# Performance work log

Measured on AMD Instinct MI355X. Metric: run time of the kernel, lower is better.

Reference implementation:

```python
import jax, jax.numpy as jnp
import numpy as np

B, N, E = 8, 10000, 320000
IN_DIM, E_H, E_OUT, N_OUT = 16, 32, 22, 16


def setup_inputs() -> dict:
    key = jax.random.key(0)
    ks = jax.random.split(key, 8)
    x = jax.random.uniform(ks[0], (B, N, IN_DIM), dtype=jnp.float32)
    edge_index = jax.random.randint(ks[1], (2, E), 0, N, dtype=jnp.int64)
    # edge_attr: col 0 = city_dist (keep strictly positive), col 1 = city_direc
    ea = jax.random.uniform(ks[2], (E, 2), dtype=jnp.float32)
    edge_attr = jnp.stack([ea[:, 0] * 100.0 + 1.0, ea[:, 1] * 360.0], axis=-1)
    wind_min = jnp.array([0.0, 0.0], dtype=jnp.float32)
    wind_max = jnp.array([15.0, 360.0], dtype=jnp.float32)
    W1 = jax.random.normal(ks[3], (2 * IN_DIM + 2 + 1, E_H), dtype=jnp.float32) * 0.1
    b1 = jnp.zeros((E_H,), dtype=jnp.float32)
    W2 = jax.random.normal(ks[4], (E_H, E_OUT), dtype=jnp.float32) * 0.1
    b2 = jnp.zeros((E_OUT,), dtype=jnp.float32)
    Wn = jax.random.normal(ks[5], (E_OUT, N_OUT), dtype=jnp.float32) * 0.1
    bn = jnp.zeros((N_OUT,), dtype=jnp.float32)
    return {"x": x, "edge_index": edge_index, "edge_attr": edge_attr,
            "wind_min": wind_min, "wind_max": wind_max,
            "W1": W1, "b1": b1, "W2": W2, "b2": b2, "Wn": Wn, "bn": bn}


def reference(x, edge_index, edge_attr, wind_min, wind_max, W1, b1, W2, b2, Wn, bn):
    edge_src = edge_index[0]
    edge_tgt = edge_index[1]
    n_nodes = x.shape[1]

    node_src = x[:, edge_src]      # [B, E, F]
    node_tgt = x[:, edge_tgt]      # [B, E, F]

    # de-normalize the last two features (wind speed, wind direction)
    src_wind = node_src[..., -2:] * (wind_max - wind_min) + wind_min
    src_speed = src_wind[..., 0]   # [B, E]
    src_direc = src_wind[..., 1]   # [B, E]

    city_dist = edge_attr[:, 0]    # [E]
    city_direc = edge_attr[:, 1]   # [E]

    theta = jnp.abs(city_direc[None, :] - src_direc)
    edge_weight = jax.nn.relu(src_speed * jnp.cos(theta) / city_dist[None, :])  # [B, E]

    ea_min = edge_attr.min(axis=0)
    ea_max = edge_attr.max(axis=0)
    ea_norm = (edge_attr - ea_min) / (ea_max - ea_min)  # [E, 2]
    ea_norm_b = jnp.broadcast_to(ea_norm[None], (x.shape[0],) + ea_norm.shape)

    feat = jnp.concatenate([node_src, node_tgt, ea_norm_b, edge_weight[..., None]], axis=-1)  # [B, E, 35]

    h = jax.nn.sigmoid(feat @ W1 + b1)   # [B, E, 32]
    e = jax.nn.sigmoid(h @ W2 + b2)      # [B, E, 22]

    # scatter_add to target nodes, scatter_add of negated messages to source nodes
    agg = jnp.zeros((x.shape[0], n_nodes, e.shape[-1]), dtype=e.dtype)
    agg = agg.at[:, edge_tgt].add(e)
    agg = agg.at[:, edge_src].add(-e)

    return jax.nn.sigmoid(agg @ Wn + bn)  # [B, N, out_dim]
```

## Files before the change

kernel.cpp:

```cpp
#include <hip/hip_runtime.h>
#include <math.h>

#define BB 8
#define NN 10000
#define EE 320000
#define NCHUNK 128
#define CHSZ (EE / NCHUNK)
#define LOG2E 1.44269504088896340736f

#define OFF_MM   0
#define PK_W2P   16
#define PK_WNP   368
#define PK_W1S   544
#define PK_B1S   576
#define PK_B2S   608
#define OFF_WIND 640
#define OFF_ECS  160640
#define OFF_PRE1 800640
#define OFF_PRE2 3360640
#define OFF_OFFP 5920640
#define OFF_TOT  5940642
#define OFF_MMP  5960642
#define OFF_CNTC 5961154
#define OFF_LST  8521154
#define OFF_G    9161168

typedef _Float16 half2_t __attribute__((ext_vector_type(2)));
typedef __fp16 fp16v2_t __attribute__((ext_vector_type(2)));

__device__ __forceinline__ float rcpf(float x) {
#if __has_builtin(__builtin_amdgcn_rcpf)
    return __builtin_amdgcn_rcpf(x);
#else
    return __fdividef(1.0f, x);
#endif
}

__device__ __forceinline__ half2_t pkh2(float a, float b) {
#if __has_builtin(__builtin_amdgcn_cvt_pkrtz)
    union { fp16v2_t t; half2_t h; } u;
    u.t = __builtin_amdgcn_cvt_pkrtz(a, b);
    return u.h;
#else
    half2_t r; r.x = (_Float16)a; r.y = (_Float16)b; return r;
#endif
}

__device__ __forceinline__ float fdot2(half2_t a, half2_t b, float c) {
#if __has_builtin(__builtin_amdgcn_fdot2)
    return __builtin_amdgcn_fdot2(a, b, c, false);
#else
    return (float)a.x * (float)b.x + (float)a.y * (float)b.y + c;
#endif
}

__device__ __forceinline__ float sig2(float xs) {
    return rcpf(1.0f + exp2f(-xs));
}

__device__ __forceinline__ float sigmf(float x) {
    return __fdividef(1.0f, 1.0f + __expf(-x));
}

union h2f { half2_t h; float f; };

__global__ __launch_bounds__(512) void pack_kernel(const float* __restrict__ W1,
                                                   const float* __restrict__ b1,
                                                   const float* __restrict__ W2,
                                                   const float* __restrict__ b2,
                                                   const float* __restrict__ Wn,
                                                   float* __restrict__ ws) {
    int t = threadIdx.x;
    if (t < 352) {
        int j2 = t / 22, k = t % 22;
        h2f u; u.h = pkh2(W2[(2 * j2) * 22 + k] * LOG2E, W2[(2 * j2 + 1) * 22 + k] * LOG2E);
        ws[PK_W2P + t] = u.f;
    }
    if (t < 176) {
        int k2 = t / 16, i = t % 16;
        h2f u; u.h = pkh2(Wn[(2 * k2) * 16 + i], Wn[(2 * k2 + 1) * 16 + i]);
        ws[PK_WNP + t] = u.f;
    }
    if (t < 32) {
        ws[PK_W1S + t] = W1[34 * 32 + t] * LOG2E;
        ws[PK_B1S + t] = b1[t] * LOG2E;
    }
    if (t < 22) ws[PK_B2S + t] = b2[t] * LOG2E;
}

__global__ __launch_bounds__(256) void count_kernel(const int* __restrict__ ei,
                                                    const float* __restrict__ ea,
                                                    unsigned* __restrict__ cntc,
                                                    float* __restrict__ mmpart) {
    __shared__ unsigned hist[NN];
    __shared__ float mred[4][4];
    const int c = blockIdx.x, a = blockIdx.y, tid = threadIdx.x;
    for (int i = tid; i < NN; i += 256) hist[i] = 0u;
    __syncthreads();
    const int e0 = c * CHSZ;
    float n0 = 3.4e38f, n1 = 3.4e38f, x0 = 0.f, x1 = 0.f;
    for (int k = tid; k < CHSZ; k += 256) {
        int v = ei[(size_t)a * EE + e0 + k];
        atomicAdd(&hist[v], 1u);
        if (a == 0) {
            float2 av = ((const float2*)ea)[e0 + k];
            n0 = fminf(n0, av.x); x0 = fmaxf(x0, av.x);
            n1 = fminf(n1, av.y); x1 = fmaxf(x1, av.y);
        }
    }
    __syncthreads();
    unsigned* dst = cntc + ((size_t)a * NCHUNK + c) * NN;
    for (int i = tid; i < NN; i += 256) dst[i] = hist[i];
    if (a == 0) {
        #pragma unroll
        for (int off = 32; off >= 1; off >>= 1) {
            n0 = fminf(n0, __shfl_xor(n0, off)); n1 = fminf(n1, __shfl_xor(n1, off));
            x0 = fmaxf(x0, __shfl_xor(x0, off)); x1 = fmaxf(x1, __shfl_xor(x1, off));
        }
        int w = tid >> 6;
        if ((tid & 63) == 0) { mred[w][0] = n0; mred[w][1] = n1; mred[w][2] = x0; mred[w][3] = x1; }
        __syncthreads();
        if (tid == 0) {
            mmpart[c * 4 + 0] = fminf(fminf(mred[0][0], mred[1][0]), fminf(mred[2][0], mred[3][0]));
            mmpart[c * 4 + 1] = fminf(fminf(mred[0][1], mred[1][1]), fminf(mred[2][1], mred[3][1]));
            mmpart[c * 4 + 2] = fmaxf(fmaxf(mred[0][2], mred[1][2]), fmaxf(mred[2][2], mred[3][2]));
            mmpart[c * 4 + 3] = fmaxf(fmaxf(mred[0][3], mred[1][3]), fmaxf(mred[2][3], mred[3][3]));
        }
    }
}

__global__ __launch_bounds__(256) void tot_kernel(const unsigned* __restrict__ cntc,
                                                  unsigned* __restrict__ tot) {
    int v = blockIdx.x * 256 + threadIdx.x;
    int a = blockIdx.y;
    if (v >= NN) return;
    const unsigned* base = cntc + (size_t)a * NCHUNK * NN;
    unsigned s = 0;
    for (int c = 0; c < NCHUNK; c++) s += base[(size_t)c * NN + v];
    tot[a * NN + v] = s;
}

__global__ __launch_bounds__(1024) void scan_kernel(const unsigned* __restrict__ tot,
                                                    const float* __restrict__ mmpart,
                                                    unsigned* __restrict__ offp,
                                                    float* __restrict__ mmo) {
    __shared__ unsigned ts[1024];
    int t = threadIdx.x;
    if (t < 64) {
        float n0 = fminf(mmpart[4 * t + 0], mmpart[4 * (t + 64) + 0]);
        float n1 = fminf(mmpart[4 * t + 1], mmpart[4 * (t + 64) + 1]);
        float x0 = fmaxf(mmpart[4 * t + 2], mmpart[4 * (t + 64) + 2]);
        float x1 = fmaxf(mmpart[4 * t + 3], mmpart[4 * (t + 64) + 3]);
        #pragma unroll
        for (int off = 32; off >= 1; off >>= 1) {
            n0 = fminf(n0, __shfl_xor(n0, off)); n1 = fminf(n1, __shfl_xor(n1, off));
            x0 = fmaxf(x0, __shfl_xor(x0, off)); x1 = fmaxf(x1, __shfl_xor(x1, off));
        }
        if (t == 0) {
            mmo[0] = n0; mmo[1] = n1;
            mmo[2] = __fdividef(LOG2E, x0 - n0);
            mmo[3] = __fdividef(LOG2E, x1 - n1);
        }
    }
    const int CH = 10;
    for (int a = 0; a < 2; a++) {
        const unsigned* c = tot + a * NN;
        unsigned* off = offp + a * (NN + 1);
        unsigned s = 0;
        int i0 = t * CH;
        #pragma unroll
        for (int k = 0; k < CH; k++) { int i = i0 + k; if (i < NN) s += c[i]; }
        ts[t] = s;
        __syncthreads();
        for (int d = 1; d < 1024; d <<= 1) {
            unsigned v = (t >= d) ? ts[t - d] : 0u;
            __syncthreads();
            ts[t] += v;
            __syncthreads();
        }
        unsigned run = ts[t] - s;
        #pragma unroll
        for (int k = 0; k < CH; k++) {
            int i = i0 + k;
            if (i < NN) { unsigned cv = c[i]; off[i] = run; run += cv; }
        }
        if (t == 1023) off[NN] = ts[1023];
        __syncthreads();
    }
}

__global__ __launch_bounds__(256) void base_kernel(unsigned* __restrict__ cntc,
                                                   const unsigned* __restrict__ offp) {
    int v = blockIdx.x * 256 + threadIdx.x;
    int a = blockIdx.y;
    if (v >= NN) return;
    unsigned run = offp[a * (NN + 1) + v];
    unsigned* base = cntc + (size_t)a * NCHUNK * NN;
    for (int c = 0; c < NCHUNK; c++) {
        unsigned cv = base[(size_t)c * NN + v];
        base[(size_t)c * NN + v] = run;
        run += cv;
    }
}

__global__ __launch_bounds__(256) void fill_kernel(const int* __restrict__ ei,
                                                   const unsigned* __restrict__ cntc,
                                                   unsigned* __restrict__ lst) {
    __shared__ unsigned cur[NN];
    const int c = blockIdx.x, a = blockIdx.y, tid = threadIdx.x;
    const unsigned* bs = cntc + ((size_t)a * NCHUNK + c) * NN;
    for (int i = tid; i < NN; i += 256) cur[i] = bs[i];
    __syncthreads();
    const int e0 = c * CHSZ;
    for (int k = tid; k < CHSZ; k += 256) {
        int e = e0 + k;
        int v = ei[(size_t)a * EE + e];
        unsigned p = atomicAdd(&cur[v], 1u);
        lst[(size_t)a * EE + p] = (unsigned)e;
    }
}

__global__ __launch_bounds__(256) void node_pre(const float* __restrict__ x,
                                                const float* __restrict__ W1,
                                                const float* __restrict__ wmin,
                                                const float* __restrict__ wmax,
                                                float* __restrict__ pre1,
                                                float* __restrict__ pre2,
                                                float* __restrict__ wind) {
    int id = blockIdx.x * 256 + threadIdx.x;
    if (id >= BB * NN) return;
    float xv[16];
    const float4* xp = (const float4*)(x + (size_t)id * 16);
    #pragma unroll
    for (int q = 0; q < 4; q++) {
        float4 v = xp[q];
        xv[4 * q + 0] = v.x; xv[4 * q + 1] = v.y;
        xv[4 * q + 2] = v.z; xv[4 * q + 3] = v.w;
    }
    float s1[32], s2[32];
    #pragma unroll
    for (int j = 0; j < 32; j++) { s1[j] = 0.f; s2[j] = 0.f; }
    #pragma unroll
    for (int r = 0; r < 16; r++) {
        float xr = xv[r];
        #pragma unroll
        for (int j = 0; j < 32; j++) {
            s1[j] = fmaf(xr, W1[r * 32 + j], s1[j]);
            s2[j] = fmaf(xr, W1[(16 + r) * 32 + j], s2[j]);
        }
    }
    float4* o1 = (float4*)(pre1 + (size_t)id * 32);
    float4* o2 = (float4*)(pre2 + (size_t)id * 32);
    #pragma unroll
    for (int q = 0; q < 8; q++) {
        o1[q] = make_float4(s1[4*q] * LOG2E, s1[4*q+1] * LOG2E, s1[4*q+2] * LOG2E, s1[4*q+3] * LOG2E);
        o2[q] = make_float4(s2[4*q] * LOG2E, s2[4*q+1] * LOG2E, s2[4*q+2] * LOG2E, s2[4*q+3] * LOG2E);
    }
    float sp = xv[14] * (wmax[0] - wmin[0]) + wmin[0];
    float dr = xv[15] * (wmax[1] - wmin[1]) + wmin[1];
    float sv, cv;
    sincosf(dr, &sv, &cv);
    ((float2*)wind)[id] = make_float2(sp * cv, sp * sv);
}

__global__ __launch_bounds__(256) void edge_pre(const float* __restrict__ ea,
                                                float* __restrict__ ecs) {
    int e = blockIdx.x * 256 + threadIdx.x;
    float2 av = ((const float2*)ea)[e];
    float sv, cv;
    sincosf(av.y, &sv, &cv);
    float rd = __fdividef(1.0f, av.x);
    ((float2*)ecs)[e] = make_float2(cv * rd, sv * rd);
}

__global__ __launch_bounds__(256) void edge_mlp(const int* __restrict__ ei,
                                                const float* __restrict__ ea,
                                                const float* __restrict__ ecs,
                                                const float* __restrict__ pre1,
                                                const float* __restrict__ pre2,
                                                const float* __restrict__ wind,
                                                const float* __restrict__ mmo,
                                                const float* __restrict__ W1,
                                                const float* __restrict__ wsf,
                                                float* __restrict__ gbuf,
                                                int b0, int nb) {
    __shared__ float gs[256 * 17];

    const int tid = threadIdx.x;
    const int e = blockIdx.x * 256 + tid;
    const int brel = blockIdx.y;
    const int b = b0 + brel;

    const int src = ei[e];
    const int tgt = ei[EE + e];
    const float2 eav = ((const float2*)ea)[e];
    const float2 ec = ((const float2*)ecs)[e];
    const float2 wv = ((const float2*)wind)[(size_t)b * NN + src];

    float ew = fmaxf(wv.x * ec.x + wv.y * ec.y, 0.f);
    float ean0 = (eav.x - mmo[0]) * mmo[2];
    float ean1 = (eav.y - mmo[1]) * mmo[3];

    const float* w1s = wsf + PK_W1S;
    const float* b1s = wsf + PK_B1S;
    const float* b2s = wsf + PK_B2S;
    const half2_t* W2p = (const half2_t*)(wsf + PK_W2P);
    const half2_t* Wnp = (const half2_t*)(wsf + PK_WNP);

    half2_t hp[16];
    const float4* p1 = (const float4*)(pre1 + ((size_t)b * NN + src) * 32);
    const float4* p2 = (const float4*)(pre2 + ((size_t)b * NN + tgt) * 32);
    #pragma unroll
    for (int q = 0; q < 8; q++) {
        float4 a = p1[q];
        float4 c = p2[q];
        float s0 = a.x + c.x, s1 = a.y + c.y, s2 = a.z + c.z, s3 = a.w + c.w;
        float h0, h1, h2, h3;
        {
            int j = 4 * q;
            h0 = sig2(s0 + ean0 * W1[32*32 + j+0] + ean1 * W1[33*32 + j+0] + ew * w1s[j+0] + b1s[j+0]);
            h1 = sig2(s1 + ean0 * W1[32*32 + j+1] + ean1 * W1[33*32 + j+1] + ew * w1s[j+1] + b1s[j+1]);
            h2 = sig2(s2 + ean0 * W1[32*32 + j+2] + ean1 * W1[33*32 + j+2] + ew * w1s[j+2] + b1s[j+2]);
            h3 = sig2(s3 + ean0 * W1[32*32 + j+3] + ean1 * W1[33*32 + j+3] + ew * w1s[j+3] + b1s[j+3]);
        }
        hp[2 * q]     = pkh2(h0, h1);
        hp[2 * q + 1] = pkh2(h2, h3);
    }

    float ef[22];
    #pragma unroll
    for (int k = 0; k < 22; k++) ef[k] = b2s[k];
    #pragma unroll
    for (int j2 = 0; j2 < 16; j2++) {
        #pragma unroll
        for (int k = 0; k < 22; k++) ef[k] = fdot2(hp[j2], W2p[j2 * 22 + k], ef[k]);
    }
    half2_t efp[11];
    #pragma unroll
    for (int k2 = 0; k2 < 11; k2++) {
        float e0 = sig2(ef[2 * k2]);
        float e1 = sig2(ef[2 * k2 + 1]);
        efp[k2] = pkh2(e0, e1);
    }

    float gg[16];
    #pragma unroll
    for (int i = 0; i < 16; i++) gg[i] = 0.f;
    #pragma unroll
    for (int k2 = 0; k2 < 11; k2++) {
        #pragma unroll
        for (int i = 0; i < 16; i++) gg[i] = fdot2(efp[k2], Wnp[k2 * 16 + i], gg[i]);
    }

    #pragma unroll
    for (int i = 0; i < 16; i++) gs[tid * 17 + i] = gg[i];
    __syncthreads();

    const int c = tid & 15;
    const int base = tid >> 4;
    const size_t ebase = (size_t)blockIdx.x * 256;
    #pragma unroll
    for (int p = 0; p < 16; p++) {
        int s = base + p * 16;
        gbuf[((ebase + s) * (size_t)nb + brel) * 16 + c] = gs[s * 17 + c];
    }
}

__global__ __launch_bounds__(256) void gather_kernel(const unsigned* __restrict__ offp,
                                                     const unsigned* __restrict__ lst,
                                                     const float* __restrict__ gbuf,
                                                     const float* __restrict__ bn,
                                                     float* __restrict__ out,
                                                     int b0, int nb, int npb, int lgper) {
    int tid = threadIdx.x;
    int n = blockIdx.x * npb + (tid >> lgper);
    int rem = tid & ((1 << lgper) - 1);
    int bi = rem >> 4;
    int c = rem & 15;

    unsigned s0 = offp[n], s1 = offp[n + 1];
    unsigned t0 = offp[NN + 1 + n], t1 = offp[NN + 1 + n + 1];

    float acc = 0.f;
    for (unsigned k = t0; k < t1; k++) {
        int e = (int)lst[EE + k];
        acc += gbuf[((size_t)e * nb + bi) * 16 + c];
    }
    for (unsigned k = s0; k < s1; k++) {
        int e = (int)lst[k];
        acc -= gbuf[((size_t)e * nb + bi) * 16 + c];
    }
    out[((size_t)(b0 + bi) * NN + n) * 16 + c] = sigmf(acc + bn[c]);
}

extern "C" void kernel_launch(void* const* d_in, const int* in_sizes, int n_in,
                              void* d_out, int out_size, void* d_ws, size_t ws_size,
                              hipStream_t stream) {
    const float* x    = (const float*)d_in[0];
    const int*   ei   = (const int*)d_in[1];
    const float* ea   = (const float*)d_in[2];
    const float* wmin = (const float*)d_in[3];
    const float* wmax = (const float*)d_in[4];
    const float* W1   = (const float*)d_in[5];
    const float* b1   = (const float*)d_in[6];
    const float* W2   = (const float*)d_in[7];
    const float* b2   = (const float*)d_in[8];
    const float* Wn   = (const float*)d_in[9];
    const float* bn   = (const float*)d_in[10];
    float* out = (float*)d_out;

    float* ws       = (float*)d_ws;
    float* mmo      = ws + OFF_MM;
    float* wind     = ws + OFF_WIND;
    float* ecs      = ws + OFF_ECS;
    float* pre1     = ws + OFF_PRE1;
    float* pre2     = ws + OFF_PRE2;
    unsigned* offp  = (unsigned*)(ws + OFF_OFFP);
    unsigned* tot   = (unsigned*)(ws + OFF_TOT);
    float* mmpart   = ws + OFF_MMP;
    unsigned* cntc  = (unsigned*)(ws + OFF_CNTC);
    unsigned* lst   = (unsigned*)(ws + OFF_LST);
    float* gbuf     = ws + OFF_G;

    int nb = 8;
    while (nb > 1 && ((size_t)OFF_G + (size_t)nb * EE * 16) * 4ull > ws_size) nb >>= 1;
    if (((size_t)OFF_G + (size_t)nb * EE * 16) * 4ull > ws_size) return;

    pack_kernel<<<1, 512, 0, stream>>>(W1, b1, W2, b2, Wn, ws);
    node_pre<<<(BB * NN + 255) / 256, 256, 0, stream>>>(x, W1, wmin, wmax, pre1, pre2, wind);
    edge_pre<<<EE / 256, 256, 0, stream>>>(ea, ecs);

    count_kernel<<<dim3(NCHUNK, 2), 256, 0, stream>>>(ei, ea, cntc, mmpart);
    tot_kernel<<<dim3((NN + 255) / 256, 2), 256, 0, stream>>>(cntc, tot);
    scan_kernel<<<1, 1024, 0, stream>>>(tot, mmpart, offp, mmo);
    base_kernel<<<dim3((NN + 255) / 256, 2), 256, 0, stream>>>(cntc, offp);
    fill_kernel<<<dim3(NCHUNK, 2), 256, 0, stream>>>(ei, cntc, lst);

    int lgnb = (nb == 8) ? 3 : (nb == 4) ? 2 : (nb == 2) ? 1 : 0;
    int per = 16 * nb;
    int npb = 256 / per;
    int lgper = 4 + lgnb;
    for (int bc = 0; bc < BB; bc += nb) {
        edge_mlp<<<dim3(EE / 256, nb), 256, 0, stream>>>(ei, ea, ecs, pre1, pre2, wind,
                                                         mmo, W1, ws, gbuf, bc, nb);
        gather_kernel<<<NN / npb, 256, 0, stream>>>(offp, lst, gbuf, bn, out,
                                                    bc, nb, npb, lgper);
    }
}
```

Baseline: 428.6 us.

## Scatter edge messages into CSR-sorted slots and split chunk prefix sums into groups

```diff
diff --git a/kernel.cpp b/kernel.cpp
--- a/kernel.cpp
+++ b/kernel.cpp
@@ -6,6 +6,8 @@
 #define EE 320000
 #define NCHUNK 128
 #define CHSZ (EE / NCHUNK)
+#define NGRP 8
+#define GCH (NCHUNK / NGRP)
 #define LOG2E 1.44269504088896340736f
 
 #define OFF_MM   0
@@ -19,11 +21,12 @@
 #define OFF_PRE1 800640
 #define OFF_PRE2 3360640
 #define OFF_OFFP 5920640
-#define OFF_TOT  5940642
-#define OFF_MMP  5960642
-#define OFF_CNTC 5961154
-#define OFF_LST  8521154
-#define OFF_G    9161168
+#define OFF_MMP  5940642
+#define OFF_TOT8 5941154
+#define OFF_GB   6101154
+#define OFF_CNTC 6261154
+#define OFF_POS  8821154
+#define OFF_S    9461156
 
 typedef _Float16 half2_t __attribute__((ext_vector_type(2)));
 typedef __fp16 fp16v2_t __attribute__((ext_vector_type(2)));
@@ -129,20 +132,22 @@
     }
 }
 
-__global__ __launch_bounds__(256) void tot_kernel(const unsigned* __restrict__ cntc,
-                                                  unsigned* __restrict__ tot) {
+__global__ __launch_bounds__(256) void tot8_kernel(const unsigned* __restrict__ cntc,
+                                                   unsigned* __restrict__ tot8) {
     int v = blockIdx.x * 256 + threadIdx.x;
-    int a = blockIdx.y;
+    int a = blockIdx.y, q = blockIdx.z;
     if (v >= NN) return;
-    const unsigned* base = cntc + (size_t)a * NCHUNK * NN;
+    const unsigned* base = cntc + (size_t)a * NCHUNK * NN + (size_t)q * GCH * NN;
     unsigned s = 0;
-    for (int c = 0; c < NCHUNK; c++) s += base[(size_t)c * NN + v];
-    tot[a * NN + v] = s;
-}
-
-__global__ __launch_bounds__(1024) void scan_kernel(const unsigned* __restrict__ tot,
+    #pragma unroll
+    for (int c = 0; c < GCH; c++) s += base[(size_t)c * NN + v];
+    tot8[(q * 2 + a) * NN + v] = s;
+}
+
+__global__ __launch_bounds__(1024) void scan_kernel(const unsigned* __restrict__ tot8,
                                                     const float* __restrict__ mmpart,
                                                     unsigned* __restrict__ offp,
+                                                    unsigned* __restrict__ gb,
                                                     float* __restrict__ mmo) {
     __shared__ unsigned ts[1024];
     int t = threadIdx.x;
@@ -164,39 +169,54 @@
     }
     const int CH = 10;
     for (int a = 0; a < 2; a++) {
-        const unsigned* c = tot + a * NN;
-        unsigned* off = offp + a * (NN + 1);
+        unsigned tv[CH];
         unsigned s = 0;
         int i0 = t * CH;
-        #pragma unroll
-        for (int k = 0; k < CH; k++) { int i = i0 + k; if (i < NN) s += c[i]; }
+        for (int k = 0; k < CH; k++) {
+            int i = i0 + k;
+            unsigned x = 0;
+            if (i < NN) {
+                #pragma unroll
+                for (int q = 0; q < NGRP; q++) x += tot8[(q * 2 + a) * NN + i];
+            }
+            tv[k] = x; s += x;
+        }
         ts[t] = s;
         __syncthreads();
         for (int d = 1; d < 1024; d <<= 1) {
-            unsigned v = (t >= d) ? ts[t - d] : 0u;
+            unsigned u = (t >= d) ? ts[t - d] : 0u;
             __syncthreads();
-            ts[t] += v;
+            ts[t] += u;
             __syncthreads();
         }
         unsigned run = ts[t] - s;
-        #pragma unroll
         for (int k = 0; k < CH; k++) {
             int i = i0 + k;
-            if (i < NN) { unsigned cv = c[i]; off[i] = run; run += cv; }
-        }
-        if (t == 1023) off[NN] = ts[1023];
+            if (i < NN) {
+                offp[a * (NN + 1) + i] = run;
+                unsigned gq = run;
+                #pragma unroll
+                for (int q = 0; q < NGRP; q++) {
+                    gb[(q * 2 + a) * NN + i] = gq;
+                    gq += tot8[(q * 2 + a) * NN + i];
+                }
+                run += tv[k];
+            }
+        }
+        if (t == 1023) offp[a * (NN + 1) + NN] = ts[1023];
         __syncthreads();
     }
 }
 
 __global__ __launch_bounds__(256) void base_kernel(unsigned* __restrict__ cntc,
-                                                   const unsigned* __restrict__ offp) {
+                                                   const unsigned* __restrict__ gb) {
     int v = blockIdx.x * 256 + threadIdx.x;
-    int a = blockIdx.y;
+    int a = blockIdx.y, q = blockIdx.z;
     if (v >= NN) return;
-    unsigned run = offp[a * (NN + 1) + v];
-    unsigned* base = cntc + (size_t)a * NCHUNK * NN;
-    for (int c = 0; c < NCHUNK; c++) {
+    unsigned run = gb[(q * 2 + a) * NN + v];
+    unsigned* base = cntc + (size_t)a * NCHUNK * NN + (size_t)q * GCH * NN;
+    #pragma unroll
+    for (int c = 0; c < GCH; c++) {
         unsigned cv = base[(size_t)c * NN + v];
         base[(size_t)c * NN + v] = run;
         run += cv;
@@ -205,7 +225,7 @@
 
 __global__ __launch_bounds__(256) void fill_kernel(const int* __restrict__ ei,
                                                    const unsigned* __restrict__ cntc,
-                                                   unsigned* __restrict__ lst) {
+                                                   unsigned* __restrict__ pos) {
     __shared__ unsigned cur[NN];
     const int c = blockIdx.x, a = blockIdx.y, tid = threadIdx.x;
     const unsigned* bs = cntc + ((size_t)a * NCHUNK + c) * NN;
@@ -216,7 +236,7 @@
         int e = e0 + k;
         int v = ei[(size_t)a * EE + e];
         unsigned p = atomicAdd(&cur[v], 1u);
-        lst[(size_t)a * EE + p] = (unsigned)e;
+        pos[(size_t)a * EE + e] = p;
     }
 }
 
@@ -282,9 +302,11 @@
                                                 const float* __restrict__ mmo,
                                                 const float* __restrict__ W1,
                                                 const float* __restrict__ wsf,
-                                                float* __restrict__ gbuf,
+                                                const unsigned* __restrict__ pos,
+                                                float* __restrict__ sbuf,
                                                 int b0, int nb) {
     __shared__ float gs[256 * 17];
+    __shared__ unsigned sl[512];
 
     const int tid = threadIdx.x;
     const int e = blockIdx.x * 256 + tid;
@@ -296,6 +318,8 @@
     const float2 eav = ((const float2*)ea)[e];
     const float2 ec = ((const float2*)ecs)[e];
     const float2 wv = ((const float2*)wind)[(size_t)b * NN + src];
+    sl[tid] = pos[e];
+    sl[256 + tid] = EE + pos[EE + e];
 
     float ew = fmaxf(wv.x * ec.x + wv.y * ec.y, 0.f);
     float ean0 = (eav.x - mmo[0]) * mmo[2];
@@ -358,17 +382,17 @@
 
     const int c = tid & 15;
     const int base = tid >> 4;
-    const size_t ebase = (size_t)blockIdx.x * 256;
     #pragma unroll
     for (int p = 0; p < 16; p++) {
         int s = base + p * 16;
-        gbuf[((ebase + s) * (size_t)nb + brel) * 16 + c] = gs[s * 17 + c];
+        float val = gs[s * 17 + c];
+        sbuf[((size_t)sl[s] * nb + brel) * 16 + c] = -val;
+        sbuf[((size_t)sl[256 + s] * nb + brel) * 16 + c] = val;
     }
 }
 
 __global__ __launch_bounds__(256) void gather_kernel(const unsigned* __restrict__ offp,
-                                                     const unsigned* __restrict__ lst,
-                                                     const float* __restrict__ gbuf,
+                                                     const float* __restrict__ sbuf,
                                                      const float* __restrict__ bn,
                                                      float* __restrict__ out,
                                                      int b0, int nb, int npb, int lgper) {
@@ -382,14 +406,10 @@
     unsigned t0 = offp[NN + 1 + n], t1 = offp[NN + 1 + n + 1];
 
     float acc = 0.f;
-    for (unsigned k = t0; k < t1; k++) {
-        int e = (int)lst[EE + k];
-        acc += gbuf[((size_t)e * nb + bi) * 16 + c];
-    }
-    for (unsigned k = s0; k < s1; k++) {
-        int e = (int)lst[k];
-        acc -= gbuf[((size_t)e * nb + bi) * 16 + c];
-    }
+    for (unsigned k = s0; k < s1; k++)
+        acc += sbuf[((size_t)k * nb + bi) * 16 + c];
+    for (unsigned k = t0; k < t1; k++)
+        acc += sbuf[(((size_t)EE + k) * nb + bi) * 16 + c];
     out[((size_t)(b0 + bi) * NN + n) * 16 + c] = sigmf(acc + bn[c]);
 }
 
@@ -416,25 +436,26 @@
     float* pre1     = ws + OFF_PRE1;
     float* pre2     = ws + OFF_PRE2;
     unsigned* offp  = (unsigned*)(ws + OFF_OFFP);
-    unsigned* tot   = (unsigned*)(ws + OFF_TOT);
     float* mmpart   = ws + OFF_MMP;
+    unsigned* tot8  = (unsigned*)(ws + OFF_TOT8);
+    unsigned* gb    = (unsigned*)(ws + OFF_GB);
     unsigned* cntc  = (unsigned*)(ws + OFF_CNTC);
-    unsigned* lst   = (unsigned*)(ws + OFF_LST);
-    float* gbuf     = ws + OFF_G;
+    unsigned* pos   = (unsigned*)(ws + OFF_POS);
+    float* sbuf     = ws + OFF_S;
 
     int nb = 8;
-    while (nb > 1 && ((size_t)OFF_G + (size_t)nb * EE * 16) * 4ull > ws_size) nb >>= 1;
-    if (((size_t)OFF_G + (size_t)nb * EE * 16) * 4ull > ws_size) return;
+    while (nb > 1 && ((size_t)OFF_S + (size_t)nb * 2 * EE * 16) * 4ull > ws_size) nb >>= 1;
+    if (((size_t)OFF_S + (size_t)nb * 2 * EE * 16) * 4ull > ws_size) return;
 
     pack_kernel<<<1, 512, 0, stream>>>(W1, b1, W2, b2, Wn, ws);
     node_pre<<<(BB * NN + 255) / 256, 256, 0, stream>>>(x, W1, wmin, wmax, pre1, pre2, wind);
     edge_pre<<<EE / 256, 256, 0, stream>>>(ea, ecs);
 
     count_kernel<<<dim3(NCHUNK, 2), 256, 0, stream>>>(ei, ea, cntc, mmpart);
-    tot_kernel<<<dim3((NN + 255) / 256, 2), 256, 0, stream>>>(cntc, tot);
-    scan_kernel<<<1, 1024, 0, stream>>>(tot, mmpart, offp, mmo);
-    base_kernel<<<dim3((NN + 255) / 256, 2), 256, 0, stream>>>(cntc, offp);
-    fill_kernel<<<dim3(NCHUNK, 2), 256, 0, stream>>>(ei, cntc, lst);
+    tot8_kernel<<<dim3((NN + 255) / 256, 2, NGRP), 256, 0, stream>>>(cntc, tot8);
+    scan_kernel<<<1, 1024, 0, stream>>>(tot8, mmpart, offp, gb, mmo);
+    base_kernel<<<dim3((NN + 255) / 256, 2, NGRP), 256, 0, stream>>>(cntc, gb);
+    fill_kernel<<<dim3(NCHUNK, 2), 256, 0, stream>>>(ei, cntc, pos);
 
     int lgnb = (nb == 8) ? 3 : (nb == 4) ? 2 : (nb == 2) ? 1 : 0;
     int per = 16 * nb;
@@ -442,8 +463,7 @@
     int lgper = 4 + lgnb;
     for (int bc = 0; bc < BB; bc += nb) {
         edge_mlp<<<dim3(EE / 256, nb), 256, 0, stream>>>(ei, ea, ecs, pre1, pre2, wind,
-                                                         mmo, W1, ws, gbuf, bc, nb);
-        gather_kernel<<<NN / npb, 256, 0, stream>>>(offp, lst, gbuf, bn, out,
-                                                    bc, nb, npb, lgper);
-    }
-}
+                                                         mmo, W1, ws, pos, sbuf, bc, nb);
+        gather_kernel<<<NN / npb, 256, 0, stream>>>(offp, sbuf, bn, out, bc, nb, npb, lgper);
+    }
+}
```

New measurement: 567.5 us. +32.4%, slower.
